# Optimization experiments

Hardware: AMD Instinct MI355X
Metric: run time of the kernel (lower is better)

Reference implementation:

```python
import jax, jax.numpy as jnp
import numpy as np

EPS = 1e-5
SLOPE = 0.2


def _conv_bn_lrelu(x, w, b, g, be, m, v):
    # 1x1 conv: (B,C,H,W) x (O,C) -> (B,O,H,W), then BN (inference) + LeakyReLU(0.2)
    y = jnp.einsum('bchw,oc->bohw', x, w) + b[None, :, None, None]
    y = g[None, :, None, None] * (y - m[None, :, None, None]) * jax.lax.rsqrt(v[None, :, None, None] + EPS) + be[None, :, None, None]
    return jnp.where(y >= 0, y, SLOPE * y)


def setup_inputs() -> dict:
    key = jax.random.key(0)
    ks = jax.random.split(key, 20)
    B, C, H, W = 8, 64, 256, 256
    d = {}
    d['x'] = jax.random.normal(ks[0], (B, C, H, W), dtype=jnp.float32)
    d['w1'] = jax.random.normal(ks[1], (1, C), dtype=jnp.float32) * 0.1
    d['b1'] = jax.random.normal(ks[2], (1,), dtype=jnp.float32)
    d['g1'] = jax.random.uniform(ks[3], (1,), dtype=jnp.float32) + 0.5
    d['be1'] = jax.random.normal(ks[4], (1,), dtype=jnp.float32)
    d['m1'] = jax.random.normal(ks[5], (1,), dtype=jnp.float32)
    d['v1'] = jax.random.uniform(ks[6], (1,), dtype=jnp.float32) + 0.5
    d['wA'] = jax.random.normal(ks[7], (C, C), dtype=jnp.float32) * 0.1
    d['bA'] = jax.random.normal(ks[8], (C,), dtype=jnp.float32)
    d['gA'] = jax.random.uniform(ks[9], (C,), dtype=jnp.float32) + 0.5
    d['beA'] = jax.random.normal(ks[10], (C,), dtype=jnp.float32)
    d['mA'] = jax.random.normal(ks[11], (C,), dtype=jnp.float32)
    d['vA'] = jax.random.uniform(ks[12], (C,), dtype=jnp.float32) + 0.5
    d['wO'] = jax.random.normal(ks[13], (C, C), dtype=jnp.float32) * 0.1
    d['bO'] = jax.random.normal(ks[14], (C,), dtype=jnp.float32)
    d['gO'] = jax.random.uniform(ks[15], (C,), dtype=jnp.float32) + 0.5
    d['beO'] = jax.random.normal(ks[16], (C,), dtype=jnp.float32)
    d['mO'] = jax.random.normal(ks[17], (C,), dtype=jnp.float32)
    d['vO'] = jax.random.uniform(ks[18], (C,), dtype=jnp.float32) + 0.5
    return d


def reference(x, w1, b1, g1, be1, m1, v1, wA, bA, gA, beA, mA, vA, wO, bO, gO, beO, mO, vO):
    B, C, H, W = x.shape
    # Branch 1: C->1 conv + BN + LeakyReLU, squeeze channel -> (B,H,W)
    C1 = _conv_bn_lrelu(x, w1, b1, g1, be1, m1, v1)[:, 0]  # (B,H,W)
    C1_t = jnp.swapaxes(C1, 1, 2)                           # (B,W,H)
    S1 = jax.nn.softmax(jnp.matmul(C1, C1_t), axis=-1)      # (B,H,H)
    S2 = jax.nn.softmax(jnp.matmul(C1_t, C1), axis=-1)      # (B,W,W)
    # Branch 2: C->C conv + BN + LeakyReLU
    C2 = _conv_bn_lrelu(x, wA, bA, gA, beA, mA, vA)         # (B,C,H,W)
    # Raw row-major reshapes as in the torch code (mixes channel and spatial dims)
    R1 = C2.reshape(B, H, C * W)
    R2 = C2.reshape(B, W, C * H)
    R3 = jnp.matmul(S1, R1).reshape(B, C, H, W)
    R4 = jnp.matmul(S2, R2).reshape(B, C, H, W)
    C3 = _conv_bn_lrelu(R3 + R4, wO, bO, gO, beO, mO, vO)
    out = C2 + C3
    return (out, S1, S2)
```

## Files before the change

kernel.cpp:

```cpp
#include <hip/hip_runtime.h>


#define EPS 1e-5f

typedef __attribute__((ext_vector_type(8))) short bf16x8;
typedef __attribute__((ext_vector_type(4))) float f32x4;

__device__ __forceinline__ unsigned short f2bf(float f){
  union { float f; unsigned int u; } a; a.f = f;
  return (unsigned short)((a.u + 0x7fffu + ((a.u >> 16) & 1u)) >> 16);
}
__device__ __forceinline__ float lrelu(float y){ return y >= 0.f ? y : 0.2f * y; }
__device__ __forceinline__ bf16x8 cvt8(const float* p){
  float4 a = *(const float4*)p;
  float4 b = *(const float4*)(p + 4);
  bf16x8 r;
  r[0] = (short)f2bf(a.x); r[1] = (short)f2bf(a.y); r[2] = (short)f2bf(a.z); r[3] = (short)f2bf(a.w);
  r[4] = (short)f2bf(b.x); r[5] = (short)f2bf(b.y); r[6] = (short)f2bf(b.z); r[7] = (short)f2bf(b.w);
  return r;
}

__global__ __launch_bounds__(256) void k1_c1(
    const float* __restrict__ x, const float* __restrict__ w1,
    const float* __restrict__ pb1, const float* __restrict__ pg1,
    const float* __restrict__ pbe1, const float* __restrict__ pm1,
    const float* __restrict__ pv1,
    float* __restrict__ C1)
{
  const int blk = blockIdx.x;
  const int b = blk >> 6;
  const int n0 = (blk & 63) << 10;
  const int t = threadIdx.x;
  __shared__ float w1s[64];
  if (t < 64) w1s[t] = w1[t];
  __syncthreads();
  const float* xb = x + ((size_t)b << 22);
  const int n = n0 + (t << 2);
  float4 d = {0.f, 0.f, 0.f, 0.f};
  #pragma unroll 16
  for (int c = 0; c < 64; c++){
    const float4 xv = *(const float4*)(xb + ((size_t)c << 16) + n);
    const float wv = w1s[c];
    d.x = fmaf(xv.x, wv, d.x); d.y = fmaf(xv.y, wv, d.y);
    d.z = fmaf(xv.z, wv, d.z); d.w = fmaf(xv.w, wv, d.w);
  }
  const float s1 = pg1[0] * rsqrtf(pv1[0] + EPS);
  const float t1 = (pb1[0] - pm1[0]) * s1 + pbe1[0];
  float4 o;
  o.x = lrelu(d.x * s1 + t1); o.y = lrelu(d.y * s1 + t1);
  o.z = lrelu(d.z * s1 + t1); o.w = lrelu(d.w * s1 + t1);
  *(float4*)(C1 + (b << 16) + n) = o;
}

__global__ __launch_bounds__(256) void k2_gram(const float* __restrict__ C1, float* __restrict__ G)
{
  const int bx = blockIdx.x;
  const int b = bx >> 5;
  const int which = (bx >> 4) & 1;
  const int tile = bx & 15;
  const int i0 = (tile >> 2) << 6, j0 = (tile & 3) << 6;
  const float* Cb = C1 + (b << 16);
  __shared__ float Al[32][68];
  __shared__ float Bl[32][68];
  const int t = threadIdx.x;
  const int tx = t & 15, ty = t >> 4;
  float acc[4][4];
  #pragma unroll
  for (int i = 0; i < 4; i++)
    #pragma unroll
    for (int j = 0; j < 4; j++) acc[i][j] = 0.f;

  for (int kc = 0; kc < 8; kc++){
    const int k0 = kc << 5;
    __syncthreads();
    if (which == 0){
      const int i = t & 63, kq = t >> 6;
      const float* pa = Cb + (i0 + i)*256 + k0 + kq*8;
      const float* pb = Cb + (j0 + i)*256 + k0 + kq*8;
      #pragma unroll
      for (int u = 0; u < 8; u++){ Al[kq*8+u][i] = pa[u]; Bl[kq*8+u][i] = pb[u]; }
    } else {
      const int k = t >> 3, i8 = (t & 7) << 3;
      const float* pa = Cb + (k0 + k)*256 + i0 + i8;
      const float* pb = Cb + (k0 + k)*256 + j0 + i8;
      *(float4*)&Al[k][i8]   = *(const float4*)pa;
      *(float4*)&Al[k][i8+4] = *(const float4*)(pa+4);
      *(float4*)&Bl[k][i8]   = *(const float4*)pb;
      *(float4*)&Bl[k][i8+4] = *(const float4*)(pb+4);
    }
    __syncthreads();
    #pragma unroll 4
    for (int k = 0; k < 32; k++){
      float4 a4 = *(const float4*)&Al[k][ty << 2];
      float4 b4 = *(const float4*)&Bl[k][tx << 2];
      float av[4] = {a4.x, a4.y, a4.z, a4.w};
      float bw[4] = {b4.x, b4.y, b4.z, b4.w};
      #pragma unroll
      for (int ii = 0; ii < 4; ii++)
        #pragma unroll
        for (int jj = 0; jj < 4; jj++)
          acc[ii][jj] = fmaf(av[ii], bw[jj], acc[ii][jj]);
    }
  }
  float* Go = G + ((size_t)(which*8 + b) << 16);
  #pragma unroll
  for (int r = 0; r < 4; r++){
    float4 o4 = {acc[r][0], acc[r][1], acc[r][2], acc[r][3]};
    *(float4*)&Go[(i0 + (ty<<2) + r)*256 + j0 + (tx<<2)] = o4;
  }
}

__global__ __launch_bounds__(256) void k2_softmax(const float* __restrict__ G,
    float* __restrict__ S1o, float* __restrict__ S2o,
    unsigned short* __restrict__ Ssum2)
{
  const int bx = blockIdx.x;
  const int b = bx >> 8, i = bx & 255;
  const int j = threadIdx.x;
  const float v1 = G[((size_t)b << 16) + i*256 + j];
  const float v2 = G[((size_t)(8 + b) << 16) + i*256 + j];
  __shared__ float sm[4], sm2[4], ss[4], ss2[4];
  float a1 = v1, a2 = v2;
  #pragma unroll
  for (int off = 32; off > 0; off >>= 1){
    a1 = fmaxf(a1, __shfl_xor(a1, off));
    a2 = fmaxf(a2, __shfl_xor(a2, off));
  }
  const int wv = j >> 6;
  if ((j & 63) == 0){ sm[wv] = a1; sm2[wv] = a2; }
  __syncthreads();
  const float m1v = fmaxf(fmaxf(sm[0], sm[1]), fmaxf(sm[2], sm[3]));
  const float m2v = fmaxf(fmaxf(sm2[0], sm2[1]), fmaxf(sm2[2], sm2[3]));
  float e1 = __expf(v1 - m1v), e2 = __expf(v2 - m2v);
  float s1 = e1, s2 = e2;
  #pragma unroll
  for (int off = 32; off > 0; off >>= 1){
    s1 += __shfl_xor(s1, off);
    s2 += __shfl_xor(s2, off);
  }
  if ((j & 63) == 0){ ss[wv] = s1; ss2[wv] = s2; }
  __syncthreads();
  const float d1 = ss[0]+ss[1]+ss[2]+ss[3];
  const float d2 = ss2[0]+ss2[1]+ss2[2]+ss2[3];
  const float S1v = e1 / d1, S2v = e2 / d2;
  S1o[((size_t)b << 16) + i*256 + j] = S1v;
  S2o[((size_t)b << 16) + i*256 + j] = S2v;
  const int ip = ((i & 3) << 6) | (i >> 2);
  const int kp = ((j & 3) << 6) | (j >> 2);
  Ssum2[((size_t)b << 16) + ip*256 + kp] = f2bf(S1v + S2v);
}

__global__ __launch_bounds__(256, 4) void k3_main(
    const float* __restrict__ x,
    const float* __restrict__ wA, const float* __restrict__ pbA,
    const float* __restrict__ pgA, const float* __restrict__ pbeA,
    const float* __restrict__ pmA, const float* __restrict__ pvA,
    const unsigned short* __restrict__ Ssum2,
    const float* __restrict__ wO, const float* __restrict__ pbO,
    const float* __restrict__ pgO, const float* __restrict__ pbeO,
    const float* __restrict__ pmO, const float* __restrict__ pvO,
    float* __restrict__ out)
{
  __shared__ unsigned short XL[128][72];
  __shared__ float sAl[64], tAl[64], sOl[64], tOl[64];
  const int blk = blockIdx.x;
  const int b  = blk >> 9;
  const int j0 = (blk & 511) << 5;
  const int t = threadIdx.x;
  const int lane = t & 63, wv = t >> 6;
  const int m = lane & 15, q = lane >> 4;

  if (t < 64){
    const float sA = pgA[t] * rsqrtf(pvA[t] + EPS);
    sAl[t] = sA; tAl[t] = (pbA[t] - pmA[t]) * sA + pbeA[t];
    const float sO = pgO[t] * rsqrtf(pvO[t] + EPS);
    sOl[t] = sO; tOl[t] = (pbO[t] - pmO[t]) * sO + pbeO[t];
  }

  {
    const float* xs = x + ((size_t)b << 22) + ((size_t)lane << 16) + (wv << 14) + j0;
    #pragma unroll
    for (int i = 0; i < 8; i++){
      const float4 xv = *(const float4*)(xs + 4*i);
      const int s = 32*wv + 4*i;
      XL[s+0][lane] = f2bf(xv.x);
      XL[s+1][lane] = f2bf(xv.y);
      XL[s+2][lane] = f2bf(xv.z);
      XL[s+3][lane] = f2bf(xv.w);
    }
  }
  __syncthreads();

  float sAv[4], tAv[4];
  #pragma unroll
  for (int ot = 0; ot < 4; ot++){ sAv[ot] = sAl[16*ot + m]; tAv[ot] = tAl[16*ot + m]; }

  bf16x8 wfrA[4][2];
  #pragma unroll
  for (int ot = 0; ot < 4; ot++)
    #pragma unroll
    for (int ks = 0; ks < 2; ks++)
      wfrA[ot][ks] = cvt8(wA + (16*ot + m)*64 + ks*32 + q*8);

  const f32x4 vzero = {0.f, 0.f, 0.f, 0.f};
  f32x4 c2r[2][4];
  #pragma unroll
  for (int i = 0; i < 2; i++)
    #pragma unroll
    for (int j = 0; j < 4; j++) c2r[i][j] = vzero;

  #pragma unroll
  for (int ks = 0; ks < 2; ks++)
    #pragma unroll
    for (int nt = 0; nt < 2; nt++){
      const bf16x8 af = *(const bf16x8*)&XL[32*wv + 16*nt + m][ks*32 + q*8];
      #pragma unroll
      for (int ot = 0; ot < 4; ot++)
        c2r[nt][ot] = __builtin_amdgcn_mfma_f32_16x16x32_bf16(af, wfrA[ot][ks], c2r[nt][ot], 0, 0, 0);
    }

  #pragma unroll
  for (int nt = 0; nt < 2; nt++)
    #pragma unroll
    for (int ot = 0; ot < 4; ot++){
      #pragma unroll
      for (int r = 0; r < 4; r++){
        const float v = lrelu(c2r[nt][ot][r] * sAv[ot] + tAv[ot]);
        c2r[nt][ot][r] = v;
        XL[32*wv + 16*nt + 4*q + r][16*ot + m] = f2bf(v);
      }
    }
  __syncthreads();

  const unsigned short* Sb = Ssum2 + ((size_t)b << 16);
  f32x4 accT[4][2];
  #pragma unroll
  for (int i = 0; i < 4; i++)
    #pragma unroll
    for (int j = 0; j < 2; j++) accT[i][j] = vzero;

  #pragma unroll
  for (int ks = 0; ks < 8; ks++){
    const int kk = ks*32 + q*8;
    const int rk = kk >> 6;
    const int c0 = kk & 63;
    bf16x8 af[4], bv[2];
    #pragma unroll
    for (int it = 0; it < 4; it++)
      af[it] = *(const bf16x8*)(Sb + (64*wv + 16*it + m)*256 + kk);
    #pragma unroll
    for (int jt = 0; jt < 2; jt++)
      bv[jt] = *(const bf16x8*)&XL[(rk << 5) + 16*jt + m][c0];
    #pragma unroll
    for (int it = 0; it < 4; it++)
      #pragma unroll
      for (int jt = 0; jt < 2; jt++)
        accT[it][jt] = __builtin_amdgcn_mfma_f32_16x16x32_bf16(af[it], bv[jt], accT[it][jt], 0, 0, 0);
  }
  __syncthreads();

  #pragma unroll
  for (int it = 0; it < 4; it++)
    #pragma unroll
    for (int jt = 0; jt < 2; jt++){
      uint2 pk;
      pk.x = (unsigned)f2bf(accT[it][jt][0]) | ((unsigned)f2bf(accT[it][jt][1]) << 16);
      pk.y = (unsigned)f2bf(accT[it][jt][2]) | ((unsigned)f2bf(accT[it][jt][3]) << 16);
      *(uint2*)&XL[32*wv + 16*jt + m][16*it + 4*q] = pk;
    }

  bf16x8 wfrO[4][2];
  #pragma unroll
  for (int ct = 0; ct < 4; ct++)
    #pragma unroll
    for (int k2 = 0; k2 < 2; k2++)
      wfrO[ct][k2] = cvt8(wO + (16*ct + m)*64 + k2*32 + q*8);

  f32x4 acc2[2][4];
  #pragma unroll
  for (int i = 0; i < 2; i++)
    #pragma unroll
    for (int j = 0; j < 4; j++) acc2[i][j] = vzero;

  #pragma unroll
  for (int k2 = 0; k2 < 2; k2++)
    #pragma unroll
    for (int stl = 0; stl < 2; stl++){
      const bf16x8 afT = *(const bf16x8*)&XL[32*wv + 16*stl + m][k2*32 + q*8];
      #pragma unroll
      for (int ct = 0; ct < 4; ct++)
        acc2[stl][ct] = __builtin_amdgcn_mfma_f32_16x16x32_bf16(afT, wfrO[ct][k2], acc2[stl][ct], 0, 0, 0);
    }

  float sOv[4], tOv[4];
  #pragma unroll
  for (int ct = 0; ct < 4; ct++){ sOv[ct] = sOl[16*ct + m]; tOv[ct] = tOl[16*ct + m]; }

  const size_t outB = ((size_t)b << 22);
  #pragma unroll
  for (int stl = 0; stl < 2; stl++)
    #pragma unroll
    for (int ct = 0; ct < 4; ct++){
      const int cout = 16*ct + m;
      const int ng0 = (wv << 14) + j0 + 16*stl + 4*q;
      float* po = out + outB + ((size_t)cout << 16) + ng0;
      float4 pk;
      pk.x = c2r[stl][ct][0] + lrelu(acc2[stl][ct][0] * sOv[ct] + tOv[ct]);
      pk.y = c2r[stl][ct][1] + lrelu(acc2[stl][ct][1] * sOv[ct] + tOv[ct]);
      pk.z = c2r[stl][ct][2] + lrelu(acc2[stl][ct][2] * sOv[ct] + tOv[ct]);
      pk.w = c2r[stl][ct][3] + lrelu(acc2[stl][ct][3] * sOv[ct] + tOv[ct]);
      *(float4*)po = pk;
    }
}

extern "C" void kernel_launch(void* const* d_in, const int* in_sizes, int n_in,
                              void* d_out, int out_size, void* d_ws, size_t ws_size,
                              hipStream_t stream) {
  const float* x   = (const float*)d_in[0];
  const float* w1  = (const float*)d_in[1];
  const float* b1  = (const float*)d_in[2];
  const float* g1  = (const float*)d_in[3];
  const float* be1 = (const float*)d_in[4];
  const float* m1  = (const float*)d_in[5];
  const float* v1  = (const float*)d_in[6];
  const float* wA  = (const float*)d_in[7];
  const float* bA  = (const float*)d_in[8];
  const float* gA  = (const float*)d_in[9];
  const float* beA = (const float*)d_in[10];
  const float* mA  = (const float*)d_in[11];
  const float* vA  = (const float*)d_in[12];
  const float* wO  = (const float*)d_in[13];
  const float* bO  = (const float*)d_in[14];
  const float* gO  = (const float*)d_in[15];
  const float* beO = (const float*)d_in[16];
  const float* mO  = (const float*)d_in[17];
  const float* vO  = (const float*)d_in[18];

  float* out = (float*)d_out;

  char* ws = (char*)d_ws;
  float* C1             = (float*)(ws);
  float* G              = (float*)(ws + (size_t)(2u << 20));
  unsigned short* Ssum2 = (unsigned short*)(ws + (size_t)(6u << 20));

  k1_c1<<<dim3(512), dim3(256), 0, stream>>>(x, w1, b1, g1, be1, m1, v1, C1);
  k2_gram<<<dim3(256), dim3(256), 0, stream>>>(C1, G);
  k2_softmax<<<dim3(2048), dim3(256), 0, stream>>>(G, out + 33554432u, out + 34078720u, Ssum2);
  k3_main<<<dim3(4096), dim3(256), 0, stream>>>(x, wA, bA, gA, beA, mA, vA, Ssum2,
                                                wO, bO, gO, beO, mO, vO, out);
}
```

Before: 447.5 us.

## Split-K the gram kernel and widen main kernel blocks to share S loads

The gram kernel now splits its K dimension into four slices across 4x more blocks, writing partial products into the output buffer as scratch, and the softmax kernel sums the four partials before normalising. The main kernel uses 512-thread blocks covering 64 spatial columns, so pairs of waves share each S row tile and the XL tile is reused across twice the columns. This is meant to fill more CUs in the small gram step and halve redundant S reads in the main kernel. The cost is extra partial-sum traffic, reuse of the output region as scratch before it is overwritten, and higher per-block LDS and register pressure.

```diff
diff --git a/kernel.cpp b/kernel.cpp
--- a/kernel.cpp
+++ b/kernel.cpp
@@ -52,12 +52,13 @@
   *(float4*)(C1 + (b << 16) + n) = o;
 }
 
-__global__ __launch_bounds__(256) void k2_gram(const float* __restrict__ C1, float* __restrict__ G)
+__global__ __launch_bounds__(256) void k2_gram(const float* __restrict__ C1, float* __restrict__ P)
 {
   const int bx = blockIdx.x;
-  const int b = bx >> 5;
-  const int which = (bx >> 4) & 1;
-  const int tile = bx & 15;
+  const int kh = bx & 3;
+  const int tile = (bx >> 2) & 15;
+  const int which = (bx >> 6) & 1;
+  const int b = bx >> 7;
   const int i0 = (tile >> 2) << 6, j0 = (tile & 3) << 6;
   const float* Cb = C1 + (b << 16);
   __shared__ float Al[32][68];
@@ -70,8 +71,8 @@
     #pragma unroll
     for (int j = 0; j < 4; j++) acc[i][j] = 0.f;
 
-  for (int kc = 0; kc < 8; kc++){
-    const int k0 = kc << 5;
+  for (int kc = 0; kc < 2; kc++){
+    const int k0 = (kh << 6) + (kc << 5);
     __syncthreads();
     if (which == 0){
       const int i = t & 63, kq = t >> 6;
@@ -102,7 +103,7 @@
           acc[ii][jj] = fmaf(av[ii], bw[jj], acc[ii][jj]);
     }
   }
-  float* Go = G + ((size_t)(which*8 + b) << 16);
+  float* Go = P + ((size_t)((kh << 4) + which*8 + b) << 16);
   #pragma unroll
   for (int r = 0; r < 4; r++){
     float4 o4 = {acc[r][0], acc[r][1], acc[r][2], acc[r][3]};
@@ -110,15 +111,19 @@
   }
 }
 
-__global__ __launch_bounds__(256) void k2_softmax(const float* __restrict__ G,
+__global__ __launch_bounds__(256) void k2_softmax(const float* __restrict__ P,
     float* __restrict__ S1o, float* __restrict__ S2o,
     unsigned short* __restrict__ Ssum2)
 {
   const int bx = blockIdx.x;
   const int b = bx >> 8, i = bx & 255;
   const int j = threadIdx.x;
-  const float v1 = G[((size_t)b << 16) + i*256 + j];
-  const float v2 = G[((size_t)(8 + b) << 16) + i*256 + j];
+  float v1 = 0.f, v2 = 0.f;
+  #pragma unroll
+  for (int kh = 0; kh < 4; kh++){
+    v1 += P[((size_t)((kh << 4) + b) << 16) + i*256 + j];
+    v2 += P[((size_t)((kh << 4) + 8 + b) << 16) + i*256 + j];
+  }
   __shared__ float sm[4], sm2[4], ss[4], ss2[4];
   float a1 = v1, a2 = v2;
   #pragma unroll
@@ -150,7 +155,7 @@
   Ssum2[((size_t)b << 16) + ip*256 + kp] = f2bf(S1v + S2v);
 }
 
-__global__ __launch_bounds__(256, 4) void k3_main(
+__global__ __launch_bounds__(512, 3) void k3_main(
     const float* __restrict__ x,
     const float* __restrict__ wA, const float* __restrict__ pbA,
     const float* __restrict__ pgA, const float* __restrict__ pbeA,
@@ -161,14 +166,16 @@
     const float* __restrict__ pmO, const float* __restrict__ pvO,
     float* __restrict__ out)
 {
-  __shared__ unsigned short XL[128][72];
+  __shared__ unsigned short XL[256][72];
   __shared__ float sAl[64], tAl[64], sOl[64], tOl[64];
   const int blk = blockIdx.x;
-  const int b  = blk >> 9;
-  const int j0 = (blk & 511) << 5;
+  const int b  = blk >> 8;
+  const int j0 = (blk & 255) << 6;
   const int t = threadIdx.x;
   const int lane = t & 63, wv = t >> 6;
-  const int m = lane & 15, q = lane >> 4;
+  const int m = lane & 15, ql = lane >> 4;
+  const int qo = wv >> 1;
+  const int jh = (wv & 1) << 5;
 
   if (t < 64){
     const float sA = pgA[t] * rsqrtf(pvA[t] + EPS);
@@ -178,7 +185,7 @@
   }
 
   {
-    const float* xs = x + ((size_t)b << 22) + ((size_t)lane << 16) + (wv << 14) + j0;
+    const float* xs = x + ((size_t)b << 22) + ((size_t)lane << 16) + (qo << 14) + j0 + jh;
     #pragma unroll
     for (int i = 0; i < 8; i++){
       const float4 xv = *(const float4*)(xs + 4*i);
@@ -200,7 +207,7 @@
   for (int ot = 0; ot < 4; ot++)
     #pragma unroll
     for (int ks = 0; ks < 2; ks++)
-      wfrA[ot][ks] = cvt8(wA + (16*ot + m)*64 + ks*32 + q*8);
+      wfrA[ot][ks] = cvt8(wA + (16*ot + m)*64 + ks*32 + ql*8);
 
   const f32x4 vzero = {0.f, 0.f, 0.f, 0.f};
   f32x4 c2r[2][4];
@@ -213,7 +220,7 @@
   for (int ks = 0; ks < 2; ks++)
     #pragma unroll
     for (int nt = 0; nt < 2; nt++){
-      const bf16x8 af = *(const bf16x8*)&XL[32*wv + 16*nt + m][ks*32 + q*8];
+      const bf16x8 af = *(const bf16x8*)&XL[32*wv + 16*nt + m][ks*32 + ql*8];
       #pragma unroll
       for (int ot = 0; ot < 4; ot++)
         c2r[nt][ot] = __builtin_amdgcn_mfma_f32_16x16x32_bf16(af, wfrA[ot][ks], c2r[nt][ot], 0, 0, 0);
@@ -227,7 +234,7 @@
       for (int r = 0; r < 4; r++){
         const float v = lrelu(c2r[nt][ot][r] * sAv[ot] + tAv[ot]);
         c2r[nt][ot][r] = v;
-        XL[32*wv + 16*nt + 4*q + r][16*ot + m] = f2bf(v);
+        XL[32*wv + 16*nt + 4*ql + r][16*ot + m] = f2bf(v);
       }
     }
   __syncthreads();
@@ -241,16 +248,16 @@
 
   #pragma unroll
   for (int ks = 0; ks < 8; ks++){
-    const int kk = ks*32 + q*8;
+    const int kk = ks*32 + ql*8;
     const int rk = kk >> 6;
     const int c0 = kk & 63;
     bf16x8 af[4], bv[2];
     #pragma unroll
     for (int it = 0; it < 4; it++)
-      af[it] = *(const bf16x8*)(Sb + (64*wv + 16*it + m)*256 + kk);
+      af[it] = *(const bf16x8*)(Sb + (64*qo + 16*it + m)*256 + kk);
     #pragma unroll
     for (int jt = 0; jt < 2; jt++)
-      bv[jt] = *(const bf16x8*)&XL[(rk << 5) + 16*jt + m][c0];
+      bv[jt] = *(const bf16x8*)&XL[(rk << 6) + jh + 16*jt + m][c0];
     #pragma unroll
     for (int it = 0; it < 4; it++)
       #pragma unroll
@@ -266,7 +273,7 @@
       uint2 pk;
       pk.x = (unsigned)f2bf(accT[it][jt][0]) | ((unsigned)f2bf(accT[it][jt][1]) << 16);
       pk.y = (unsigned)f2bf(accT[it][jt][2]) | ((unsigned)f2bf(accT[it][jt][3]) << 16);
-      *(uint2*)&XL[32*wv + 16*jt + m][16*it + 4*q] = pk;
+      *(uint2*)&XL[32*wv + 16*jt + m][16*it + 4*ql] = pk;
     }
 
   bf16x8 wfrO[4][2];
@@ -274,7 +281,7 @@
   for (int ct = 0; ct < 4; ct++)
     #pragma unroll
     for (int k2 = 0; k2 < 2; k2++)
-      wfrO[ct][k2] = cvt8(wO + (16*ct + m)*64 + k2*32 + q*8);
+      wfrO[ct][k2] = cvt8(wO + (16*ct + m)*64 + k2*32 + ql*8);
 
   f32x4 acc2[2][4];
   #pragma unroll
@@ -286,7 +293,7 @@
   for (int k2 = 0; k2 < 2; k2++)
     #pragma unroll
     for (int stl = 0; stl < 2; stl++){
-      const bf16x8 afT = *(const bf16x8*)&XL[32*wv + 16*stl + m][k2*32 + q*8];
+      const bf16x8 afT = *(const bf16x8*)&XL[32*wv + 16*stl + m][k2*32 + ql*8];
       #pragma unroll
       for (int ct = 0; ct < 4; ct++)
         acc2[stl][ct] = __builtin_amdgcn_mfma_f32_16x16x32_bf16(afT, wfrO[ct][k2], acc2[stl][ct], 0, 0, 0);
@@ -302,7 +309,7 @@
     #pragma unroll
     for (int ct = 0; ct < 4; ct++){
       const int cout = 16*ct + m;
-      const int ng0 = (wv << 14) + j0 + 16*stl + 4*q;
+      const int ng0 = (qo << 14) + j0 + jh + 16*stl + 4*ql;
       float* po = out + outB + ((size_t)cout << 16) + ng0;
       float4 pk;
       pk.x = c2r[stl][ct][0] + lrelu(acc2[stl][ct][0] * sOv[ct] + tOv[ct]);
@@ -340,12 +347,11 @@
 
   char* ws = (char*)d_ws;
   float* C1             = (float*)(ws);
-  float* G              = (float*)(ws + (size_t)(2u << 20));
   unsigned short* Ssum2 = (unsigned short*)(ws + (size_t)(6u << 20));
 
   k1_c1<<<dim3(512), dim3(256), 0, stream>>>(x, w1, b1, g1, be1, m1, v1, C1);
-  k2_gram<<<dim3(256), dim3(256), 0, stream>>>(C1, G);
-  k2_softmax<<<dim3(2048), dim3(256), 0, stream>>>(G, out + 33554432u, out + 34078720u, Ssum2);
-  k3_main<<<dim3(4096), dim3(256), 0, stream>>>(x, wA, bA, gA, beA, mA, vA, Ssum2,
+  k2_gram<<<dim3(1024), dim3(256), 0, stream>>>(C1, out);
+  k2_softmax<<<dim3(2048), dim3(256), 0, stream>>>(out, out + 33554432u, out + 34078720u, Ssum2);
+  k3_main<<<dim3(2048), dim3(512), 0, stream>>>(x, wA, bA, gA, beA, mA, vA, Ssum2,
                                                 wO, bO, gO, beO, mO, vO, out);
 }
```

Measured after the change: 433.3 us. 1.03x faster.
